# Kernel optimization log

Hardware: AMD Instinct MI355X
Metric: run time of the kernel (lower is better)

The kernel has to match this reference:

```python
import jax, jax.numpy as jnp
import numpy as np

S = 1024; VOCAB = 100000; EMB = 300
POS_SZ = 64; CHAR_E = 50; CHAR_ENC = 128; WLEN = 16
NCHARS = 100; NPOSTAG = 50; NPOSITIONS = 1024
D = EMB + 3 * POS_SZ + CHAR_ENC  # word_rep_size = 620
BIH = 128   # per-direction LSTM hidden (bilstm_hidden_size // 2)
TLH = 256; LCC = 128; GCC = 256
NET = 8; NTAGS = 16; NREL = 16
TOKF = 2 * BIH + LCC + TLH       # 640
SENTF = 2 * TOKF + GCC           # 1536

def _p(k, shape):
    return 0.02 * jax.random.normal(k, shape, dtype=jnp.float32)

def setup_inputs():
    key = jax.random.key(0)
    ks = jax.random.split(key, 30)
    return {
        'word_inputs': jax.random.randint(ks[0], (1, S), 0, VOCAB),
        'char_inputs': jax.random.randint(ks[1], (1, S, WLEN), 0, NCHARS),
        'postag_inputs': jax.random.randint(ks[2], (1, S), 0, NPOSTAG),
        'dependency_inputs': jax.random.randint(ks[3], (1, S), 0, 64),
        'position_inputs': jax.random.randint(ks[4], (1, S), 0, NPOSITIONS),
        'topo_order': jnp.arange(S),  # children-before-parents order
        'parent': jnp.concatenate([jnp.arange(1, S), jnp.array([S])]),  # chain dep tree; root -> dummy slot S
        'pointed_token_idx': 5,
        'word_table': _p(ks[5], (VOCAB, EMB)),
        'char_table': _p(ks[6], (NCHARS, CHAR_E)),
        'char_conv_w': _p(ks[7], (CHAR_ENC, CHAR_E, 3)),
        'char_conv_b': jnp.zeros((CHAR_ENC,), jnp.float32),
        'postag_table': _p(ks[8], (NPOSTAG, POS_SZ)),
        'position_table': _p(ks[9], (NPOSITIONS, POS_SZ)),
        'lstm_f_Wx': _p(ks[10], (D, 4 * BIH)),
        'lstm_f_Wh': _p(ks[11], (BIH, 4 * BIH)),
        'lstm_f_b': jnp.zeros((4 * BIH,), jnp.float32),
        'lstm_b_Wx': _p(ks[12], (D, 4 * BIH)),
        'lstm_b_Wh': _p(ks[13], (BIH, 4 * BIH)),
        'lstm_b_b': jnp.zeros((4 * BIH,), jnp.float32),
        'word_cnn_w': _p(ks[14], (LCC, D, 3)),
        'word_cnn_b': jnp.zeros((LCC,), jnp.float32),
        'tl_Wiou': _p(ks[15], (D, 3 * TLH)),
        'tl_Uiou': _p(ks[16], (TLH, 3 * TLH)),
        'tl_biou': jnp.zeros((3 * TLH,), jnp.float32),
        'tl_Wf': _p(ks[17], (D, TLH)),
        'tl_Uf': _p(ks[18], (TLH, TLH)),
        'tl_bf': jnp.zeros((TLH,), jnp.float32),
        'sent_cnn_w': _p(ks[19], (GCC, D, 3)),
        'sent_cnn_b': jnp.zeros((GCC,), jnp.float32),
        'et_w': _p(ks[20], (GCC + TOKF, NET)),
        'et_b': jnp.zeros((NET,), jnp.float32),
        'crf_w': _p(ks[21], (SENTF, NTAGS)),
        'crf_b': jnp.zeros((NTAGS,), jnp.float32),
        'crf_trans': _p(ks[22], (NTAGS, NTAGS)),
        'rel_w': _p(ks[23], (SENTF, NREL)),
        'rel_b': jnp.zeros((NREL,), jnp.float32),
    }

def _conv1d(x, w, b):
    # x: [N, Cin, W], w: [Cout, Cin, K], padding=1 (matches nn.Conv1d(..., padding=1))
    y = jax.lax.conv_general_dilated(x, w, (1,), [(1, 1)], dimension_numbers=('NCW', 'OIW', 'NCW'))
    return y + b[None, :, None]

def _lstm(xs, Wx, Wh, b):
    H = Wh.shape[0]
    def step(carry, x):
        h, c = carry
        g = x @ Wx + h @ Wh + b
        i, f, gg, o = jnp.split(g, 4, axis=-1)
        c = jax.nn.sigmoid(f) * c + jax.nn.sigmoid(i) * jnp.tanh(gg)
        h = jax.nn.sigmoid(o) * jnp.tanh(c)
        return (h, c), h
    init = (jnp.zeros((H,), xs.dtype), jnp.zeros((H,), xs.dtype))
    _, hs = jax.lax.scan(step, init, xs)
    return hs

def _tree_lstm(x, order, parent, Wiou, Uiou, biou, Wf, Uf, bf):
    # ChildSum TreeLSTM over the whole dependency tree in topological order.
    # Equivalent to the source's per-token subtree recursion: each node's h
    # only depends on its subtree.
    Sn, H = x.shape[0], Uf.shape[0]
    xiou = x @ Wiou + biou                 # [S, 3H]
    xf = jnp.concatenate([x @ Wf + bf, jnp.zeros((1, H), x.dtype)], axis=0)  # dummy row for root's parent
    def step(carry, j):
        h, hsum, fcsum = carry
        iou = xiou[j] + hsum[j] @ Uiou
        i, o, u = jnp.split(iou, 3)
        cj = jax.nn.sigmoid(i) * jnp.tanh(u) + fcsum[j]
        hj = jax.nn.sigmoid(o) * jnp.tanh(cj)
        p = parent[j]
        f = jax.nn.sigmoid(xf[p] + hj @ Uf)  # per-child forget gate
        return (h.at[j].set(hj), hsum.at[p].add(hj), fcsum.at[p].add(f * cj)), None
    h0 = jnp.zeros((Sn, H), x.dtype)
    acc0 = jnp.zeros((Sn + 1, H), x.dtype)
    (h, _, _), _ = jax.lax.scan(step, (h0, acc0, acc0), order)
    return h

def _viterbi(emissions, trans):
    # emissions: [S, T]; trans[i, j] = score(i -> j)
    def step(score, e):
        s = score[:, None] + trans
        return jnp.max(s, axis=0) + e, jnp.argmax(s, axis=0)
    final, ptrs = jax.lax.scan(step, emissions[0], emissions[1:])
    last = jnp.argmax(final)
    def bt(tag, p):
        prev = p[tag]
        return prev, prev
    _, prevs = jax.lax.scan(bt, last, ptrs, reverse=True)
    return jnp.concatenate([prevs, last[None]])

def reference(word_inputs, char_inputs, postag_inputs, dependency_inputs, position_inputs, topo_order, parent, pointed_token_idx, word_table, char_table, char_conv_w, char_conv_b, postag_table, position_table, lstm_f_Wx, lstm_f_Wh, lstm_f_b, lstm_b_Wx, lstm_b_Wh, lstm_b_b, word_cnn_w, word_cnn_b, tl_Wiou, tl_Uiou, tl_biou, tl_Wf, tl_Uf, tl_bf, sent_cnn_w, sent_cnn_b, et_w, et_b, crf_w, crf_b, crf_trans, rel_w, rel_b):
    we = word_table[word_inputs]                                   # [1,S,EMB]
    cx = jnp.transpose(char_table[char_inputs[0]], (0, 2, 1))      # [S,CHAR_E,WLEN]
    ce = jnp.max(jax.nn.relu(_conv1d(cx, char_conv_w, char_conv_b)), axis=-1)[None]  # CharCNN -> [1,S,CHAR_ENC]
    pe = postag_table[postag_inputs]
    poe = position_table[position_inputs]
    de = position_table[dependency_inputs]                         # faithful to source bug: uses position table
    inputs = jnp.concatenate([we, ce, pe, poe, de], axis=-1)       # [1,S,D]
    x = inputs[0]
    hf = _lstm(x, lstm_f_Wx, lstm_f_Wh, lstm_f_b)
    hb = _lstm(x[::-1], lstm_b_Wx, lstm_b_Wh, lstm_b_b)[::-1]
    bilstm = jnp.concatenate([hf, hb], axis=-1)[None]              # [1,S,2*BIH]
    xc = jnp.transpose(inputs, (0, 2, 1))                          # [1,D,S]
    local_cnn = jnp.transpose(_conv1d(xc, word_cnn_w, word_cnn_b), (0, 2, 1))
    tree_h = _tree_lstm(x, topo_order, parent, tl_Wiou, tl_Uiou, tl_biou, tl_Wf, tl_Uf, tl_bf)[None]
    global_cnn = jnp.transpose(jnp.max(_conv1d(xc, sent_cnn_w, sent_cnn_b), axis=-1, keepdims=True), (0, 2, 1))  # [1,1,GCC]
    tokens_info = jnp.concatenate([bilstm, local_cnn, tree_h], axis=-1)  # [1,S,TOKF]
    ptr = tokens_info[:, pointed_token_idx, :]                     # [1,TOKF]
    ptr_info = jnp.broadcast_to(ptr[:, None, :], (1, S, TOKF))
    glob_info = jnp.broadcast_to(global_cnn, (1, S, GCC))
    sentence_encoding = jnp.concatenate([tokens_info, ptr_info, glob_info], axis=-1)  # dropout = identity (eval)
    one_vec = jnp.concatenate([global_cnn[:, 0, :], ptr], axis=-1)
    entitytype = jax.nn.softmax(one_vec @ et_w + et_b, axis=-1)
    entities = _viterbi(sentence_encoding[0] @ crf_w + crf_b, crf_trans)
    relations = jax.nn.sigmoid(sentence_encoding @ rel_w + rel_b)
    return sentence_encoding, entitytype, entities, relations
```

## Files before the change

### kernel.cpp

```cpp
#include <hip/hip_runtime.h>
#include <math.h>

#define SEQ   1024
#define DX    620
#define BIH   128
#define TLH   256
#define NTAGS 16

#define O_X      0
#define O_XGF    634880
#define O_XGB    (O_XGF + 524288)
#define O_XIOU   (O_XGB + 524288)
#define O_XF     (O_XIOU + 786432)
#define O_LCNN   (O_XF + 262400)
#define O_SCNN   (O_LCNN + 131072)
#define O_PART   (O_SCNN + 262144)
#define O_GCNN   (O_PART + 4096)
#define O_HF     (O_GCNN + 256)
#define O_HB     (O_HF + 131072)
#define O_TREEH  (O_HB + 131072)
#define O_IOUA   (O_TREEH + 262144)
#define O_FCSUM  (O_IOUA + 787200)
#define O_EMIS   (O_FCSUM + 262400)
#define O_DONE   (O_EMIS + 16384)

#define SENT 0xFFFFFFFFu

typedef float f32x4_t __attribute__((ext_vector_type(4)));

__device__ __forceinline__ float sig_f(float x){ return 1.0f/(1.0f + __expf(-x)); }
__device__ __forceinline__ float tanh_f(float x){
  float ax = fabsf(x);
  float e  = __expf(-2.0f*ax);
  float t  = (1.0f - e)/(1.0f + e);
  return x < 0.0f ? -t : t;
}
__device__ __forceinline__ int physslot(int s){ return s ^ ((s>>3)&7); }

__global__ __launch_bounds__(128) void k_embed(
    const int* __restrict__ wi, const int* __restrict__ ci,
    const int* __restrict__ postag_in, const int* __restrict__ dep_in, const int* __restrict__ pos_in,
    const float* __restrict__ word_table, const float* __restrict__ char_table,
    const float* __restrict__ ccw, const float* __restrict__ ccb,
    const float* __restrict__ postag_table, const float* __restrict__ position_table,
    float* __restrict__ x)
{
  int s = blockIdx.x;
  int tid = threadIdx.x;
  __shared__ __align__(16) float ce[50][16];
  for (int idx = tid; idx < 800; idx += 128){
    int e = idx >> 4, t = idx & 15;
    ce[e][t] = char_table[ci[s*16 + t]*50 + e];
  }
  __syncthreads();
  float* xr = x + (size_t)s*DX;
  const float* wrow = word_table + (size_t)wi[s]*300;
  for (int d = tid; d < 300; d += 128) xr[d] = wrow[d];
  {
    int oc = tid;
    const float* wp = ccw + oc*150;
    float acc[16];
    float b = ccb[oc];
    #pragma unroll
    for (int t=0;t<16;t++) acc[t] = b;
    for (int ic=0; ic<50; ic++){
      float w0 = wp[ic*3+0], w1 = wp[ic*3+1], w2 = wp[ic*3+2];
      float cv[16];
      float4 c0 = *(const float4*)&ce[ic][0];
      float4 c1 = *(const float4*)&ce[ic][4];
      float4 c2 = *(const float4*)&ce[ic][8];
      float4 c3 = *(const float4*)&ce[ic][12];
      cv[0]=c0.x;cv[1]=c0.y;cv[2]=c0.z;cv[3]=c0.w;
      cv[4]=c1.x;cv[5]=c1.y;cv[6]=c1.z;cv[7]=c1.w;
      cv[8]=c2.x;cv[9]=c2.y;cv[10]=c2.z;cv[11]=c2.w;
      cv[12]=c3.x;cv[13]=c3.y;cv[14]=c3.z;cv[15]=c3.w;
      #pragma unroll
      for (int t=0;t<16;t++){
        float a = cv[t]*w1;
        if (t > 0)  a += cv[t-1]*w0;
        if (t < 15) a += cv[t+1]*w2;
        acc[t] += a;
      }
    }
    float m = acc[0];
    #pragma unroll
    for (int t=1;t<16;t++) m = fmaxf(m, acc[t]);
    xr[300 + oc] = fmaxf(m, 0.0f);
  }
  if (tid < 64){
    int d = tid;
    xr[428 + d] = postag_table[postag_in[s]*64 + d];
    xr[492 + d] = position_table[pos_in[s]*64 + d];
    xr[556 + d] = position_table[dep_in[s]*64 + d];
  }
}

struct GemmArgs {
  const float* B[6];
  const float* bias[6];
  float*       C[6];
  int N[6]; int K[6]; int amode[6];
};

__global__ __launch_bounds__(256) void k_gemm(const float* __restrict__ x, GemmArgs ga)
{
  int z = blockIdx.z;
  int N = ga.N[z], K = ga.K[z], amode = ga.amode[z];
  int bn = blockIdx.x*64;
  if (bn >= N) return;
  int bm = blockIdx.y*64;
  const float* __restrict__ Bm = ga.B[z];
  __shared__ __align__(16) float As[20][64];
  __shared__ __align__(16) float Bs[20][64];
  int tid = threadIdx.x;
  int lane = tid & 63, kg = tid >> 6;
  int tx = tid & 15, ty = tid >> 4;
  float acc[4][4] = {{0.f}};
  for (int k0 = 0; k0 < K; k0 += 20){
    #pragma unroll
    for (int kk=0; kk<5; kk++){
      int k = kg*5 + kk;
      float av;
      if (amode == 0){
        av = x[(size_t)(bm+lane)*DX + k0 + k];
      } else {
        int kc = k0 + k;
        int d  = kc/3;
        int sh = kc - d*3 - 1;
        int row = bm + lane + sh;
        av = (row >= 0 && row < SEQ) ? x[(size_t)row*DX + d] : 0.0f;
      }
      As[k][lane] = av;
      Bs[k][lane] = (amode==0) ? Bm[(size_t)(k0+k)*N + bn + lane]
                               : Bm[(size_t)(bn+lane)*K + k0 + k];
    }
    __syncthreads();
    #pragma unroll
    for (int k=0;k<20;k++){
      float4 a = *(const float4*)&As[k][ty<<2];
      float4 b = *(const float4*)&Bs[k][tx<<2];
      acc[0][0]+=a.x*b.x; acc[0][1]+=a.x*b.y; acc[0][2]+=a.x*b.z; acc[0][3]+=a.x*b.w;
      acc[1][0]+=a.y*b.x; acc[1][1]+=a.y*b.y; acc[1][2]+=a.y*b.z; acc[1][3]+=a.y*b.w;
      acc[2][0]+=a.z*b.x; acc[2][1]+=a.z*b.y; acc[2][2]+=a.z*b.z; acc[2][3]+=a.z*b.w;
      acc[3][0]+=a.w*b.x; acc[3][1]+=a.w*b.y; acc[3][2]+=a.w*b.z; acc[3][3]+=a.w*b.w;
    }
    __syncthreads();
  }
  const float* bias = ga.bias[z];
  float* C = ga.C[z];
  float4 bb;
  bb.x = bias[bn+(tx<<2)+0]; bb.y = bias[bn+(tx<<2)+1];
  bb.z = bias[bn+(tx<<2)+2]; bb.w = bias[bn+(tx<<2)+3];
  #pragma unroll
  for (int i=0;i<4;i++){
    int row = bm + (ty<<2) + i;
    float4 o;
    o.x = acc[i][0] + bb.x; o.y = acc[i][1] + bb.y;
    o.z = acc[i][2] + bb.z; o.w = acc[i][3] + bb.w;
    *(float4*)&C[(size_t)row*N + bn + (tx<<2)] = o;
  }
}

__global__ __launch_bounds__(256) void k_gmax1(const float* __restrict__ scnn, float* __restrict__ part){
  int b = blockIdx.x, c = threadIdx.x;
  float m = -3.0e38f;
  for (int s = b*64; s < b*64 + 64; s++) m = fmaxf(m, scnn[(size_t)s*256 + c]);
  part[b*256 + c] = m;
}
__global__ __launch_bounds__(256) void k_gmax2(const float* __restrict__ part, float* __restrict__ gcnn){
  int c = threadIdx.x;
  float m = -3.0e38f;
  for (int b=0; b<16; b++) m = fmaxf(m, part[b*256 + c]);
  gcnn[c] = m;
}

__global__ __launch_bounds__(256, 1) void k_recur(
    const float* __restrict__ xg_f, const float* __restrict__ xg_b,
    const float* __restrict__ Wh_f, const float* __restrict__ Wh_b,
    const float* __restrict__ xiou, const float* __restrict__ xf,
    const float* __restrict__ Uiou, const float* __restrict__ Uf,
    const int* __restrict__ order, const int* __restrict__ parent,
    float* __restrict__ hf, float* __restrict__ hb,
    float* tree_h, float* iou_acc, float* fcsum, unsigned* done)
{
  int bid = blockIdx.x;
  int tid = threadIdx.x;

  if (bid >= 6){
    float f0 = 1.0f + (float)tid * 1e-7f, f1 = 1.1f, f2 = 1.2f, f3 = 1.3f;
    while (__hip_atomic_load(done, __ATOMIC_RELAXED, __HIP_MEMORY_SCOPE_AGENT) < 6u){
      #pragma unroll
      for (int i=0;i<256;i++){
        f0 = fmaf(f0, 0.99999988f, 1e-9f);
        f1 = fmaf(f1, 0.99999988f, 1e-9f);
        f2 = fmaf(f2, 0.99999988f, 1e-9f);
        f3 = fmaf(f3, 0.99999988f, 1e-9f);
      }
      asm volatile("" :: "v"(f0), "v"(f1), "v"(f2), "v"(f3));
    }
    return;
  }

  if (bid >= 4){
    const float* xg  = (bid == 4) ? xg_f : xg_b;
    const float* Wh  = (bid == 4) ? Wh_f : Wh_b;
    float* hout      = (bid == 4) ? hf : hb;
    int cg = tid >> 1, rg = tid & 1;
    float4 w[4][16];
    #pragma unroll
    for (int cc=0;cc<4;cc++){
      int col = cg*4 + cc;
      #pragma unroll
      for (int r4=0;r4<16;r4++){
        int row = rg*64 + r4*4;
        w[cc][r4].x = Wh[(size_t)(row+0)*512 + col];
        w[cc][r4].y = Wh[(size_t)(row+1)*512 + col];
        w[cc][r4].z = Wh[(size_t)(row+2)*512 + col];
        w[cc][r4].w = Wh[(size_t)(row+3)*512 + col];
      }
    }
    #pragma unroll
    for (int cc=0;cc<4;cc++)
      #pragma unroll
      for (int r4=0;r4<16;r4++)
        asm volatile("" : "+v"(w[cc][r4].x), "+v"(w[cc][r4].y), "+v"(w[cc][r4].z), "+v"(w[cc][r4].w));

    __shared__ __align__(16) float lhl[BIH];
    __shared__ float lcst[BIH];
    __shared__ float gl[512];
    if (tid < BIH){ lhl[tid] = 0.f; lcst[tid] = 0.f; }
    __syncthreads();
    const float4* lhl4 = (const float4*)lhl;
    float4 nxg4 = make_float4(0.f,0.f,0.f,0.f);
    if (rg == 0){
      int n0 = (bid == 4) ? 0 : (SEQ-1);
      nxg4 = *(const float4*)&xg[(size_t)n0*512 + cg*4];
    }
    for (int st=0; st<SEQ; st++){
      int n = (bid == 4) ? st : (SEQ-1-st);
      float4 xg4 = nxg4;
      if (rg == 0 && st+1 < SEQ){
        int n1 = (bid == 4) ? (st+1) : (SEQ-2-st);
        nxg4 = *(const float4*)&xg[(size_t)n1*512 + cg*4];
      }
      float acc[4] = {0.f,0.f,0.f,0.f};
      #pragma unroll
      for (int r4=0;r4<16;r4++){
        float4 h4 = lhl4[rg*16 + r4];
        #pragma unroll
        for (int cc=0;cc<4;cc++)
          acc[cc] += h4.x*w[cc][r4].x + h4.y*w[cc][r4].y + h4.z*w[cc][r4].z + h4.w*w[cc][r4].w;
      }
      #pragma unroll
      for (int cc=0;cc<4;cc++) acc[cc] += __shfl_xor(acc[cc], 1);
      if (rg == 0){
        float4 o = make_float4(acc[0]+xg4.x, acc[1]+xg4.y, acc[2]+xg4.z, acc[3]+xg4.w);
        *(float4*)&gl[cg*4] = o;
      }
      __syncthreads();
      if (tid < BIH){
        float gi = gl[tid], gf = gl[BIH+tid], gg = gl[2*BIH+tid], go = gl[3*BIH+tid];
        float c = sig_f(gf)*lcst[tid] + sig_f(gi)*tanh_f(gg);
        float h = sig_f(go)*tanh_f(c);
        lcst[tid] = c;
        lhl[tid] = h;
        hout[(size_t)n*BIH + tid] = h;
      }
      __syncthreads();
    }
    if (tid == 0) __hip_atomic_fetch_add(done, 1u, __ATOMIC_RELEASE, __HIP_MEMORY_SCOPE_AGENT);
    return;
  }

  int blk = bid;
  int cg = tid >> 3, rg = tid & 7;
  int ulo = blk*64;
  float4 w[8][8];
  #pragma unroll
  for (int cc=0;cc<8;cc++){
    int c = cg*8 + cc;
    const float* Wsrc; size_t stride; int gcol;
    if (c < 192){ Wsrc = Uiou; stride = 768; gcol = (c>>6)*TLH + ulo + (c&63); }
    else        { Wsrc = Uf;   stride = 256; gcol = ulo + (c-192); }
    #pragma unroll
    for (int r4=0;r4<8;r4++){
      int row = rg*32 + r4*4;
      w[cc][r4].x = Wsrc[(size_t)(row+0)*stride + gcol];
      w[cc][r4].y = Wsrc[(size_t)(row+1)*stride + gcol];
      w[cc][r4].z = Wsrc[(size_t)(row+2)*stride + gcol];
      w[cc][r4].w = Wsrc[(size_t)(row+3)*stride + gcol];
    }
  }
  #pragma unroll
  for (int cc=0;cc<8;cc++)
    #pragma unroll
    for (int r4=0;r4<8;r4++)
      asm volatile("" : "+v"(w[cc][r4].x), "+v"(w[cc][r4].y), "+v"(w[cc][r4].z), "+v"(w[cc][r4].w));

  __shared__ __align__(16) float hl[TLH];
  __shared__ float colsum[TLH];
  __shared__ float cprev[64];
  __shared__ int ord_l[SEQ];
  __shared__ int par_l[SEQ];
  for (int i=tid; i<SEQ; i+=256){ ord_l[i] = order[i]; par_l[i] = parent[i]; }
  __syncthreads();
  const float4* hl4 = (const float4*)hl;

  float nxi=0.f, nxo=0.f, nxu=0.f, nxf=0.f;
  if (tid < 64){
    int n0 = ord_l[0];
    int uu = ulo + tid;
    nxi = xiou[(size_t)n0*768 + uu];
    nxo = xiou[(size_t)n0*768 + 256 + uu];
    nxu = xiou[(size_t)n0*768 + 512 + uu];
  }

  for (int t=0; t<SEQ; t++){
    int n  = ord_l[t];
    int m  = (t > 0) ? ord_l[t-1] : 0;
    int pp = (t > 0) ? par_l[m] : -1;
    bool ppeq = (pp == n);

    float xi=nxi, xo=nxo, xu=nxu, xfv=nxf;
    float ac_i=0.f, ac_o=0.f, ac_u=0.f, fcn=0.f;
    float po_i=0.f, po_o=0.f, po_u=0.f, po_f=0.f;
    if (tid < 64){
      int uu = ulo + tid;
      if (t+1 < SEQ){
        int n1 = ord_l[t+1];
        nxi = xiou[(size_t)n1*768 + uu];
        nxo = xiou[(size_t)n1*768 + 256 + uu];
        nxu = xiou[(size_t)n1*768 + 512 + uu];
        nxf = xf[(size_t)par_l[n]*256 + uu];
      }
      ac_i = iou_acc[(size_t)n*768 + uu];
      ac_o = iou_acc[(size_t)n*768 + 256 + uu];
      ac_u = iou_acc[(size_t)n*768 + 512 + uu];
      fcn  = fcsum[(size_t)n*256 + uu];
      if (t > 0 && !ppeq){
        po_i = iou_acc[(size_t)pp*768 + uu];
        po_o = iou_acc[(size_t)pp*768 + 256 + uu];
        po_u = iou_acc[(size_t)pp*768 + 512 + uu];
        po_f = fcsum[(size_t)pp*256 + uu];
      }
    }

    if (t > 0){
      float acc[8] = {0.f,0.f,0.f,0.f,0.f,0.f,0.f,0.f};
      int base = rg << 3;
      #pragma unroll
      for (int r4=0;r4<8;r4++){
        float4 h4 = hl4[base + (r4 ^ rg)];
        #pragma unroll
        for (int cc=0;cc<8;cc++)
          acc[cc] += h4.x*w[cc][r4].x + h4.y*w[cc][r4].y + h4.z*w[cc][r4].z + h4.w*w[cc][r4].w;
      }
      #pragma unroll
      for (int cc=0;cc<8;cc++){
        acc[cc] += __shfl_xor(acc[cc], 1);
        acc[cc] += __shfl_xor(acc[cc], 2);
        acc[cc] += __shfl_xor(acc[cc], 4);
      }
      if (rg == 0){
        *(float4*)&colsum[cg*8]     = make_float4(acc[0], acc[1], acc[2], acc[3]);
        *(float4*)&colsum[cg*8 + 4] = make_float4(acc[4], acc[5], acc[6], acc[7]);
      }
    }
    __syncthreads();

    if (tid < 64){
      int uu = ulo + tid;
      float ai = ac_i, ao = ac_o, au = ac_u, fcs = fcn;
      if (t > 0){
        float vi = colsum[tid], vo = colsum[64+tid], vuu = colsum[128+tid], vf = colsum[192+tid];
        float fg  = sig_f(xfv + vf);
        float fcc = fg * cprev[tid];
        if (ppeq){
          ai += vi; ao += vo; au += vuu; fcs += fcc;
        } else {
          iou_acc[(size_t)pp*768 + uu]       = po_i + vi;
          iou_acc[(size_t)pp*768 + 256 + uu] = po_o + vo;
          iou_acc[(size_t)pp*768 + 512 + uu] = po_u + vuu;
          fcsum[(size_t)pp*256 + uu]         = po_f + fcc;
        }
      }
      float cc = sig_f(xi + ai)*tanh_f(xu + au) + fcs;
      float hh = sig_f(xo + ao)*tanh_f(cc);
      cprev[tid] = cc;
      int s = uu >> 2;
      hl[physslot(s)*4 + (uu & 3)] = hh;
      float* tp = &tree_h[(size_t)n*TLH + uu];
      asm volatile("global_store_dword %0, %1, off sc0 sc1" :: "v"(tp), "v"(hh) : "memory");
    } else {
      int p  = tid - 64;
      int fi = (p < ulo) ? p : p + 64;
      const unsigned* tp = (const unsigned*)(tree_h + (size_t)n*TLH + fi);
      unsigned v;
      do {
        v = __hip_atomic_load(tp, __ATOMIC_RELAXED, __HIP_MEMORY_SCOPE_AGENT);
      } while (v == SENT);
      hl[physslot(fi>>2)*4 + (fi&3)] = __uint_as_float(v);
    }
    __syncthreads();
  }
  if (tid == 0) __hip_atomic_fetch_add(done, 1u, __ATOMIC_RELEASE, __HIP_MEMORY_SCOPE_AGENT);
}

__global__ __launch_bounds__(256) void k_assemble(
    const float* __restrict__ hf, const float* __restrict__ hb,
    const float* __restrict__ lcnn, const float* __restrict__ tree_h,
    const float* __restrict__ gcnn,
    const float* __restrict__ crf_w, const float* __restrict__ crf_b,
    const float* __restrict__ rel_w, const float* __restrict__ rel_b,
    const int* __restrict__ ptk,
    float* __restrict__ se_out, float* __restrict__ emis, float* __restrict__ rel_out)
{
  int s = blockIdx.x, tid = threadIdx.x;
  int p = ptk[0];
  __shared__ float se[1536];
  for (int d = tid; d < 1536; d += 256){
    float v;
    if      (d < 128)  v = hf[(size_t)s*128 + d];
    else if (d < 256)  v = hb[(size_t)s*128 + d-128];
    else if (d < 384)  v = lcnn[(size_t)s*128 + d-256];
    else if (d < 640)  v = tree_h[(size_t)s*256 + d-384];
    else if (d < 768)  v = hf[(size_t)p*128 + d-640];
    else if (d < 896)  v = hb[(size_t)p*128 + d-768];
    else if (d < 1024) v = lcnn[(size_t)p*128 + d-896];
    else if (d < 1280) v = tree_h[(size_t)p*256 + d-1024];
    else               v = gcnn[d-1280];
    se[d] = v;
    se_out[(size_t)s*1536 + d] = v;
  }
  __syncthreads();
  int o = tid >> 3, l = tid & 7;
  const float* W = (o < 16) ? crf_w : rel_w;
  int oc = (o < 16) ? o : (o - 16);
  float a = 0.f;
  for (int k = l; k < 1536; k += 8) a += se[k]*W[(size_t)k*16 + oc];
  for (int off = 4; off; off >>= 1) a += __shfl_down(a, off, 8);
  if (l == 0){
    if (o < 16) emis[(size_t)s*16 + o] = a + crf_b[o];
    else        rel_out[(size_t)s*16 + oc] = sig_f(a + rel_b[oc]);
  }
}

__global__ __launch_bounds__(256) void k_entity(
    const float* __restrict__ hf, const float* __restrict__ hb,
    const float* __restrict__ lcnn, const float* __restrict__ tree_h,
    const float* __restrict__ gcnn,
    const float* __restrict__ et_w, const float* __restrict__ et_b,
    const int* __restrict__ ptk, float* __restrict__ out_et)
{
  __shared__ float ov[896];
  __shared__ float lg[8];
  int tid = threadIdx.x;
  int p = ptk[0];
  for (int d = tid; d < 896; d += 256){
    float v;
    if      (d < 256) v = gcnn[d];
    else if (d < 384) v = hf[(size_t)p*128 + d-256];
    else if (d < 512) v = hb[(size_t)p*128 + d-384];
    else if (d < 640) v = lcnn[(size_t)p*128 + d-512];
    else              v = tree_h[(size_t)p*256 + d-640];
    ov[d] = v;
  }
  __syncthreads();
  int o = tid >> 5, l = tid & 31;
  float a = 0.f;
  for (int k = l; k < 896; k += 32) a += ov[k]*et_w[(size_t)k*8 + o];
  for (int off = 16; off; off >>= 1) a += __shfl_down(a, off, 32);
  if (l == 0) lg[o] = a + et_b[o];
  __syncthreads();
  if (tid == 0){
    float mx = lg[0];
    for (int i=1;i<8;i++) mx = fmaxf(mx, lg[i]);
    float e[8], sum = 0.f;
    for (int i=0;i<8;i++){ e[i] = __expf(lg[i]-mx); sum += e[i]; }
    for (int i=0;i<8;i++) out_et[i] = e[i]/sum;
  }
}

__global__ __launch_bounds__(64) void k_viterbi(
    const float* __restrict__ emis, const float* __restrict__ trans, float* __restrict__ out_e)
{
  __shared__ __align__(16) float ring[64][16];
  __shared__ unsigned char ptrs[1023*16];
  __shared__ float scL[16];
  int l = threadIdx.x;
  int j = l >> 2, iq = l & 3;
  float tr0 = trans[(iq*4+0)*16 + j];
  float tr1 = trans[(iq*4+1)*16 + j];
  float tr2 = trans[(iq*4+2)*16 + j];
  float tr3 = trans[(iq*4+3)*16 + j];
  {
    const float* src = &emis[(size_t)l*16];
    float4 a = *(const float4*)(src+0), b = *(const float4*)(src+4);
    float4 c = *(const float4*)(src+8), d = *(const float4*)(src+12);
    *(float4*)&ring[l][0] = a;  *(float4*)&ring[l][4] = b;
    *(float4*)&ring[l][8] = c;  *(float4*)&ring[l][12] = d;
  }
  float cur = ring[0][j];
  float sc0 = __shfl(cur, (iq*4+0)<<2, 64);
  float sc1 = __shfl(cur, (iq*4+1)<<2, 64);
  float sc2 = __shfl(cur, (iq*4+2)<<2, 64);
  float sc3 = __shfl(cur, (iq*4+3)<<2, 64);
  float myfinal = cur;
  for (int t=1; t<1024; t++){
    if ((t & 63) == 0){
      const float* src = &emis[(size_t)(t+l)*16];
      float4 a = *(const float4*)(src+0), b = *(const float4*)(src+4);
      float4 c = *(const float4*)(src+8), d = *(const float4*)(src+12);
      int rr = (t+l) & 63;
      *(float4*)&ring[rr][0] = a;  *(float4*)&ring[rr][4] = b;
      *(float4*)&ring[rr][8] = c;  *(float4*)&ring[rr][12] = d;
    }
    float v0 = sc0 + tr0, v1 = sc1 + tr1, v2 = sc2 + tr2, v3 = sc3 + tr3;
    float best = v0; int barg = iq*4;
    if (v1 > best){ best = v1; barg = iq*4+1; }
    if (v2 > best){ best = v2; barg = iq*4+2; }
    if (v3 > best){ best = v3; barg = iq*4+3; }
    float ob = __shfl_down(best, 1, 4); int oa = __shfl_down(barg, 1, 4);
    if (ob > best){ best = ob; barg = oa; }
    ob = __shfl_down(best, 2, 4); oa = __shfl_down(barg, 2, 4);
    if (ob > best){ best = ob; barg = oa; }
    float ns = 0.f;
    if (iq == 0){
      ns = best + ring[t & 63][j];
      ptrs[(t-1)*16 + j] = (unsigned char)barg;
      myfinal = ns;
    }
    sc0 = __shfl(ns, (iq*4+0)<<2, 64);
    sc1 = __shfl(ns, (iq*4+1)<<2, 64);
    sc2 = __shfl(ns, (iq*4+2)<<2, 64);
    sc3 = __shfl(ns, (iq*4+3)<<2, 64);
  }
  if (iq == 0) scL[j] = myfinal;
  if (l == 0){
    float b = scL[0]; int last = 0;
    #pragma unroll
    for (int i=1;i<16;i++){ if (scL[i] > b){ b = scL[i]; last = i; } }
    out_e[1023] = (float)last;
    int cur2 = last;
    for (int t=1022; t>=0; t--){ cur2 = (int)ptrs[t*16 + cur2]; out_e[t] = (float)cur2; }
  }
}

extern "C" void kernel_launch(void* const* d_in, const int* in_sizes, int n_in,
                              void* d_out, int out_size, void* d_ws, size_t ws_size,
                              hipStream_t stream)
{
  (void)in_sizes; (void)n_in; (void)out_size; (void)ws_size;
  const int*   wi         = (const int*)d_in[0];
  const int*   ci         = (const int*)d_in[1];
  const int*   postag_in  = (const int*)d_in[2];
  const int*   dep_in     = (const int*)d_in[3];
  const int*   pos_in     = (const int*)d_in[4];
  const int*   order      = (const int*)d_in[5];
  const int*   parent     = (const int*)d_in[6];
  const int*   ptk        = (const int*)d_in[7];
  const float* word_table = (const float*)d_in[8];
  const float* char_table = (const float*)d_in[9];
  const float* ccw        = (const float*)d_in[10];
  const float* ccb        = (const float*)d_in[11];
  const float* postag_tab = (const float*)d_in[12];
  const float* pos_tab    = (const float*)d_in[13];
  const float* Wx_f       = (const float*)d_in[14];
  const float* Wh_f       = (const float*)d_in[15];
  const float* b_f        = (const float*)d_in[16];
  const float* Wx_b       = (const float*)d_in[17];
  const float* Wh_b       = (const float*)d_in[18];
  const float* b_b        = (const float*)d_in[19];
  const float* wcnn_w     = (const float*)d_in[20];
  const float* wcnn_b     = (const float*)d_in[21];
  const float* Wiou       = (const float*)d_in[22];
  const float* Uiou       = (const float*)d_in[23];
  const float* biou       = (const float*)d_in[24];
  const float* Wf_t       = (const float*)d_in[25];
  const float* Uf_t       = (const float*)d_in[26];
  const float* bf_t       = (const float*)d_in[27];
  const float* scnn_w     = (const float*)d_in[28];
  const float* scnn_b     = (const float*)d_in[29];
  const float* et_w       = (const float*)d_in[30];
  const float* et_b       = (const float*)d_in[31];
  const float* crf_w      = (const float*)d_in[32];
  const float* crf_b      = (const float*)d_in[33];
  const float* crf_trans  = (const float*)d_in[34];
  const float* rel_w      = (const float*)d_in[35];
  const float* rel_b      = (const float*)d_in[36];

  float* ws = (float*)d_ws;
  float* x      = ws + O_X;
  float* xg_f   = ws + O_XGF;
  float* xg_b   = ws + O_XGB;
  float* xiou   = ws + O_XIOU;
  float* xf     = ws + O_XF;
  float* lcnn   = ws + O_LCNN;
  float* scnn   = ws + O_SCNN;
  float* part   = ws + O_PART;
  float* gcnn   = ws + O_GCNN;
  float* hf     = ws + O_HF;
  float* hb     = ws + O_HB;
  float* tree_h = ws + O_TREEH;
  float* iou_acc= ws + O_IOUA;
  float* fcsum  = ws + O_FCSUM;
  float* emis   = ws + O_EMIS;
  unsigned* done= (unsigned*)(ws + O_DONE);

  float* outF     = (float*)d_out;
  float* se_out   = outF;
  float* et_out   = outF + 1572864;
  float* ent_out  = outF + 1572872;
  float* rel_out  = outF + 1573896;

  hipMemsetAsync(xf, 0, (size_t)1025*256*sizeof(float), stream);
  hipMemsetAsync(iou_acc, 0, ((size_t)1025*768 + 1025*256)*sizeof(float), stream);
  hipMemsetAsync(tree_h, 0xFF, (size_t)1024*256*sizeof(float), stream);
  hipMemsetAsync(done, 0, 64, stream);

  k_embed<<<SEQ, 128, 0, stream>>>(wi, ci, postag_in, dep_in, pos_in,
                                   word_table, char_table, ccw, ccb,
                                   postag_tab, pos_tab, x);

  GemmArgs ga;
  ga.B[0]=Wx_f;  ga.bias[0]=b_f;   ga.C[0]=xg_f; ga.N[0]=512; ga.K[0]=620;  ga.amode[0]=0;
  ga.B[1]=Wx_b;  ga.bias[1]=b_b;   ga.C[1]=xg_b; ga.N[1]=512; ga.K[1]=620;  ga.amode[1]=0;
  ga.B[2]=Wiou;  ga.bias[2]=biou;  ga.C[2]=xiou; ga.N[2]=768; ga.K[2]=620;  ga.amode[2]=0;
  ga.B[3]=Wf_t;  ga.bias[3]=bf_t;  ga.C[3]=xf;   ga.N[3]=256; ga.K[3]=620;  ga.amode[3]=0;
  ga.B[4]=wcnn_w;ga.bias[4]=wcnn_b;ga.C[4]=lcnn; ga.N[4]=128; ga.K[4]=1860; ga.amode[4]=1;
  ga.B[5]=scnn_w;ga.bias[5]=scnn_b;ga.C[5]=scnn; ga.N[5]=256; ga.K[5]=1860; ga.amode[5]=1;
  k_gemm<<<dim3(12,16,6), 256, 0, stream>>>(x, ga);

  k_gmax1<<<16, 256, 0, stream>>>(scnn, part);
  k_gmax2<<<1, 256, 0, stream>>>(part, gcnn);

  k_recur<<<64, 256, 0, stream>>>(xg_f, xg_b, Wh_f, Wh_b, xiou, xf, Uiou, Uf_t,
                                  order, parent, hf, hb, tree_h, iou_acc, fcsum, done);

  k_assemble<<<SEQ, 256, 0, stream>>>(hf, hb, lcnn, tree_h, gcnn,
                                      crf_w, crf_b, rel_w, rel_b, ptk,
                                      se_out, emis, rel_out);

  k_entity<<<1, 256, 0, stream>>>(hf, hb, lcnn, tree_h, gcnn, et_w, et_b, ptk, et_out);

  k_viterbi<<<1, 64, 0, stream>>>(emis, crf_trans, ent_out);
}
```

Measured before the change: 2.863 ms.

## Overlap conv GEMMs with recurrent kernel using idle blocks instead of spin-heaters

The two CNN convolution GEMMs (local and sentence) move out of the batched GEMM launch. They now run inside the recurrent kernel's extra blocks, which previously only spun doing dummy FMAs until the sequential LSTM and tree-LSTM blocks finished. The done counter and heater loop are gone, the tree-LSTM spin-wait gains an s_sleep backoff, and the sc0/sc1 inline-asm store becomes an agent-scope atomic store. This hides conv work behind the latency-bound recurrence. The risk is that the removed heater was keeping clocks up, and the conv blocks may contend with the recurrence for memory bandwidth.

```diff
diff --git a/kernel.cpp b/kernel.cpp
--- a/kernel.cpp
+++ b/kernel.cpp
@@ -22,11 +22,8 @@
 #define O_IOUA   (O_TREEH + 262144)
 #define O_FCSUM  (O_IOUA + 787200)
 #define O_EMIS   (O_FCSUM + 262400)
-#define O_DONE   (O_EMIS + 16384)
 
 #define SENT 0xFFFFFFFFu
-
-typedef float f32x4_t __attribute__((ext_vector_type(4)));
 
 __device__ __forceinline__ float sig_f(float x){ return 1.0f/(1.0f + __expf(-x)); }
 __device__ __forceinline__ float tanh_f(float x){
@@ -95,24 +92,13 @@
   }
 }
 
-struct GemmArgs {
-  const float* B[6];
-  const float* bias[6];
-  float*       C[6];
-  int N[6]; int K[6]; int amode[6];
-};
-
-__global__ __launch_bounds__(256) void k_gemm(const float* __restrict__ x, GemmArgs ga)
-{
-  int z = blockIdx.z;
-  int N = ga.N[z], K = ga.K[z], amode = ga.amode[z];
-  int bn = blockIdx.x*64;
-  if (bn >= N) return;
-  int bm = blockIdx.y*64;
-  const float* __restrict__ Bm = ga.B[z];
-  __shared__ __align__(16) float As[20][64];
-  __shared__ __align__(16) float Bs[20][64];
-  int tid = threadIdx.x;
+__device__ __forceinline__ void gemm_tile(
+    const float* __restrict__ x, const float* __restrict__ Bm,
+    const float* __restrict__ bias, float* __restrict__ C,
+    int N, int K, int amode, int bx, int by, int tid,
+    float (*As)[64], float (*Bs)[64])
+{
+  int bn = bx*64, bm = by*64;
   int lane = tid & 63, kg = tid >> 6;
   int tx = tid & 15, ty = tid >> 4;
   float acc[4][4] = {{0.f}};
@@ -146,8 +132,6 @@
     }
     __syncthreads();
   }
-  const float* bias = ga.bias[z];
-  float* C = ga.C[z];
   float4 bb;
   bb.x = bias[bn+(tx<<2)+0]; bb.y = bias[bn+(tx<<2)+1];
   bb.z = bias[bn+(tx<<2)+2]; bb.w = bias[bn+(tx<<2)+3];
@@ -161,6 +145,23 @@
   }
 }
 
+struct GemmArgs {
+  const float* B[4];
+  const float* bias[4];
+  float*       C[4];
+  int N[4]; int K[4];
+};
+
+__global__ __launch_bounds__(256) void k_gemm(const float* __restrict__ x, GemmArgs ga)
+{
+  __shared__ __align__(16) float As[20][64];
+  __shared__ __align__(16) float Bs[20][64];
+  int z = blockIdx.z;
+  if (blockIdx.x*64 >= ga.N[z]) return;
+  gemm_tile(x, ga.B[z], ga.bias[z], ga.C[z], ga.N[z], ga.K[z], 0,
+            blockIdx.x, blockIdx.y, threadIdx.x, As, Bs);
+}
+
 __global__ __launch_bounds__(256) void k_gmax1(const float* __restrict__ scnn, float* __restrict__ part){
   int b = blockIdx.x, c = threadIdx.x;
   float m = -3.0e38f;
@@ -181,22 +182,24 @@
     const float* __restrict__ Uiou, const float* __restrict__ Uf,
     const int* __restrict__ order, const int* __restrict__ parent,
     float* __restrict__ hf, float* __restrict__ hb,
-    float* tree_h, float* iou_acc, float* fcsum, unsigned* done)
+    float* tree_h, float* iou_acc, float* fcsum,
+    const float* __restrict__ x,
+    const float* __restrict__ wcnn_w, const float* __restrict__ wcnn_b,
+    const float* __restrict__ scnn_w, const float* __restrict__ scnn_b,
+    float* __restrict__ lcnn, float* __restrict__ scnn)
 {
   int bid = blockIdx.x;
   int tid = threadIdx.x;
 
   if (bid >= 6){
-    float f0 = 1.0f + (float)tid * 1e-7f, f1 = 1.1f, f2 = 1.2f, f3 = 1.3f;
-    while (__hip_atomic_load(done, __ATOMIC_RELAXED, __HIP_MEMORY_SCOPE_AGENT) < 6u){
-      #pragma unroll
-      for (int i=0;i<256;i++){
-        f0 = fmaf(f0, 0.99999988f, 1e-9f);
-        f1 = fmaf(f1, 0.99999988f, 1e-9f);
-        f2 = fmaf(f2, 0.99999988f, 1e-9f);
-        f3 = fmaf(f3, 0.99999988f, 1e-9f);
-      }
-      asm volatile("" :: "v"(f0), "v"(f1), "v"(f2), "v"(f3));
+    __shared__ __align__(16) float As[20][64];
+    __shared__ __align__(16) float Bs[20][64];
+    int g = bid - 6;
+    if (g < 32){
+      gemm_tile(x, wcnn_w, wcnn_b, lcnn, 128, 1860, 1, g & 1, g >> 1, tid, As, Bs);
+    } else {
+      int g2 = g - 32;
+      gemm_tile(x, scnn_w, scnn_b, scnn, 256, 1860, 1, g2 & 3, g2 >> 2, tid, As, Bs);
     }
     return;
   }
@@ -268,7 +271,6 @@
       }
       __syncthreads();
     }
-    if (tid == 0) __hip_atomic_fetch_add(done, 1u, __ATOMIC_RELEASE, __HIP_MEMORY_SCOPE_AGENT);
     return;
   }
 
@@ -389,21 +391,20 @@
       cprev[tid] = cc;
       int s = uu >> 2;
       hl[physslot(s)*4 + (uu & 3)] = hh;
-      float* tp = &tree_h[(size_t)n*TLH + uu];
-      asm volatile("global_store_dword %0, %1, off sc0 sc1" :: "v"(tp), "v"(hh) : "memory");
+      __hip_atomic_store(&tree_h[(size_t)n*TLH + uu], hh, __ATOMIC_RELAXED, __HIP_MEMORY_SCOPE_AGENT);
     } else {
       int p  = tid - 64;
       int fi = (p < ulo) ? p : p + 64;
       const unsigned* tp = (const unsigned*)(tree_h + (size_t)n*TLH + fi);
-      unsigned v;
-      do {
+      unsigned v = __hip_atomic_load(tp, __ATOMIC_RELAXED, __HIP_MEMORY_SCOPE_AGENT);
+      while (v == SENT){
+        __builtin_amdgcn_s_sleep(1);
         v = __hip_atomic_load(tp, __ATOMIC_RELAXED, __HIP_MEMORY_SCOPE_AGENT);
-      } while (v == SENT);
+      }
       hl[physslot(fi>>2)*4 + (fi&3)] = __uint_as_float(v);
     }
     __syncthreads();
   }
-  if (tid == 0) __hip_atomic_fetch_add(done, 1u, __ATOMIC_RELEASE, __HIP_MEMORY_SCOPE_AGENT);
 }
 
 __global__ __launch_bounds__(256) void k_assemble(
@@ -605,7 +606,6 @@
   float* iou_acc= ws + O_IOUA;
   float* fcsum  = ws + O_FCSUM;
   float* emis   = ws + O_EMIS;
-  unsigned* done= (unsigned*)(ws + O_DONE);
 
   float* outF     = (float*)d_out;
   float* se_out   = outF;
@@ -616,26 +616,24 @@
   hipMemsetAsync(xf, 0, (size_t)1025*256*sizeof(float), stream);
   hipMemsetAsync(iou_acc, 0, ((size_t)1025*768 + 1025*256)*sizeof(float), stream);
   hipMemsetAsync(tree_h, 0xFF, (size_t)1024*256*sizeof(float), stream);
-  hipMemsetAsync(done, 0, 64, stream);
 
   k_embed<<<SEQ, 128, 0, stream>>>(wi, ci, postag_in, dep_in, pos_in,
                                    word_table, char_table, ccw, ccb,
                                    postag_tab, pos_tab, x);
 
   GemmArgs ga;
-  ga.B[0]=Wx_f;  ga.bias[0]=b_f;   ga.C[0]=xg_f; ga.N[0]=512; ga.K[0]=620;  ga.amode[0]=0;
-  ga.B[1]=Wx_b;  ga.bias[1]=b_b;   ga.C[1]=xg_b; ga.N[1]=512; ga.K[1]=620;  ga.amode[1]=0;
-  ga.B[2]=Wiou;  ga.bias[2]=biou;  ga.C[2]=xiou; ga.N[2]=768; ga.K[2]=620;  ga.amode[2]=0;
-  ga.B[3]=Wf_t;  ga.bias[3]=bf_t;  ga.C[3]=xf;   ga.N[3]=256; ga.K[3]=620;  ga.amode[3]=0;
-  ga.B[4]=wcnn_w;ga.bias[4]=wcnn_b;ga.C[4]=lcnn; ga.N[4]=128; ga.K[4]=1860; ga.amode[4]=1;
-  ga.B[5]=scnn_w;ga.bias[5]=scnn_b;ga.C[5]=scnn; ga.N[5]=256; ga.K[5]=1860; ga.amode[5]=1;
-  k_gemm<<<dim3(12,16,6), 256, 0, stream>>>(x, ga);
+  ga.B[0]=Wx_f;  ga.bias[0]=b_f;   ga.C[0]=xg_f; ga.N[0]=512; ga.K[0]=620;
+  ga.B[1]=Wx_b;  ga.bias[1]=b_b;   ga.C[1]=xg_b; ga.N[1]=512; ga.K[1]=620;
+  ga.B[2]=Wiou;  ga.bias[2]=biou;  ga.C[2]=xiou; ga.N[2]=768; ga.K[2]=620;
+  ga.B[3]=Wf_t;  ga.bias[3]=bf_t;  ga.C[3]=xf;   ga.N[3]=256; ga.K[3]=620;
+  k_gemm<<<dim3(12,16,4), 256, 0, stream>>>(x, ga);
+
+  k_recur<<<102, 256, 0, stream>>>(xg_f, xg_b, Wh_f, Wh_b, xiou, xf, Uiou, Uf_t,
+                                   order, parent, hf, hb, tree_h, iou_acc, fcsum,
+                                   x, wcnn_w, wcnn_b, scnn_w, scnn_b, lcnn, scnn);
 
   k_gmax1<<<16, 256, 0, stream>>>(scnn, part);
   k_gmax2<<<1, 256, 0, stream>>>(part, gcnn);
-
-  k_recur<<<64, 256, 0, stream>>>(xg_f, xg_b, Wh_f, Wh_b, xiou, xf, Uiou, Uf_t,
-                                  order, parent, hf, hb, tree_h, iou_acc, fcsum, done);
 
   k_assemble<<<SEQ, 256, 0, stream>>>(hf, hb, lcnn, tree_h, gcnn,
                                       crf_w, crf_b, rel_w, rel_b, ptk,
```

New measurement: 2.762 ms. -3.5%, faster.
